# Performance work log

Hardware: AMD Instinct MI355X
Metric: run time of the kernel (lower is better)

Reference implementation:

```python
import jax, jax.numpy as jnp
import numpy as np

# dims: B batch, N nodes, E edges, C=dim_in, W=window_len, D=embed_dim, O=dim_out, K=link_len, NB=bootstrap count
B, N, E, C, W, D, O, K, NB = 16, 2000, 3000, 17, 12, 16, 256, 3, 3


def setup_inputs() -> dict:
    key = jax.random.key(0)
    ks = jax.random.split(key, 20)
    return {
        "x": jax.random.normal(ks[0], (B, N, C), jnp.float32),
        "x_window": jax.random.normal(ks[1], (B, W, N, 1), jnp.float32),
        "node_embeddings": jax.random.normal(ks[2], (N, D), jnp.float32) * 0.1,
        "fixed_adj": 0,
        "adj": jax.random.normal(ks[3], (N, N), jnp.float32),
        "stay_cost": 1,
        "jump_cost": 1,
        "ZFC_input": jax.random.normal(ks[4], (B, O // 8), jnp.float32),
        "hodge_Laplacian": jax.random.normal(ks[5], (E, E), jnp.float32) * 0.02,
        "x_e_window": jax.random.normal(ks[6], (B, W, E, 1), jnp.float32),
        "incidence_matrix": jax.random.normal(ks[7], (N, E), jnp.float32) * 0.02,
        "weights_pool": jax.random.normal(ks[8], (D, K, C, O // 4), jnp.float32) * 0.05,
        "window_weights_supra": jax.random.normal(ks[9], (D, 1, O // 8), jnp.float32) * 0.05,
        "window_weights_temporal": jax.random.normal(ks[10], (D, 1, O // 2), jnp.float32) * 0.05,
        "bias_pool": jax.random.normal(ks[11], (D, O), jnp.float32) * 0.05,
        "T_param": jax.random.normal(ks[12], (W,), jnp.float32) * 0.1,
        "lin_w": jax.random.normal(ks[13], (1, 1), jnp.float32),
        "lin_b": jax.random.normal(ks[14], (1,), jnp.float32),
        "gnn_w": jax.random.normal(ks[15], (N, N), jnp.float32) * 0.02,
        "gnn_b": jnp.zeros((N,), jnp.float32),
        "bootstrap_idx": jnp.sort(jax.random.randint(ks[16], (NB,), 0, W)),
    }


def _forward(x, x_window, ne, fixed_adj, adj, stay_cost, jump_cost, ZFC_input,
             hodge, x_e_window, inc, wp, wws_p, wwt_p, bp, Tp, lin_w, lin_b,
             gnn_w, gnn_b, bidx):
    n = ne.shape[0]
    e = hodge.shape[0]
    b = x.shape[0]
    nb = bidx.shape[0]

    # adaptive transition matrix S (diag filled with stay_cost after relu)
    S0 = jax.nn.relu(ne @ ne.T)
    ii = jnp.arange(n)
    S0 = S0.at[ii, ii].set(jnp.float32(stay_cost))
    if fixed_adj:  # static Python bool branch
        S = adj * jnp.exp(S0)
    else:
        S = jax.nn.softmax(S0, axis=1)
    # faithful to torch broadcasting: column j divided by row-sum of row j
    S = S / jnp.sum(S, axis=1)

    # diffusion support power series: [I, S, S@S, ...]
    sup = [jnp.eye(n, dtype=S.dtype), S]
    for _ in range(2, K):
        sup.append(S @ sup[-1])
    supports = jnp.stack(sup, axis=0)  # (K, N, N)

    # supra-Laplacian: hodge on diagonal blocks, jump_cost*I on strict upper blocks
    supra = (jnp.kron(jnp.eye(nb, dtype=hodge.dtype), hodge)
             + jnp.kron(jnp.triu(jnp.ones((nb, nb), hodge.dtype), 1),
                        jnp.float32(jump_cost) * jnp.eye(e, dtype=hodge.dtype)))  # (nb*E, nb*E)

    # adaptive weights/bias from node embeddings
    weights = jnp.einsum('nd,dkio->nkio', ne, wp)   # (N, K, C, O/4)
    bias = ne @ bp                                   # (N, O)

    # graph diffusion branch
    x_s = jnp.einsum('knm,bmc->bknc', supports, x).transpose(0, 2, 1, 3)  # (B,N,K,C)
    x_sconv = jnp.einsum('bnki,nkio->bno', x_s, weights)                   # (B,N,O/4)

    # supra / hypergraph branch
    wws = jnp.einsum('nd,dio->nio', ne, wws_p)                 # (N,1,O/8)
    xe = x_e_window[:, bidx].reshape(b, nb * e, 1)             # bootstrap gather
    xe = xe * lin_w[0, 0] + lin_b[0]                           # Linear(1,1)
    xes = jnp.einsum('bmi,mn->bni', xe, supra).reshape(b, nb, 1, e)
    xen = jnp.einsum('bfim,mn->bfin', xes, inc.T).reshape(b, nb, n, 1)
    x_e_n_wconv = jnp.einsum('bfni,nio->bfno', xen, wws).mean(axis=1)  # (B,N,O/8)

    # temporal window branch (einsum fuses the permute + matmul with T)
    wwt = jnp.einsum('nd,dio->nio', ne, wwt_p)                  # (N,1,O/2)
    x_wconv_t = jnp.einsum('btni,nio,t->bno', x_window, wwt, Tp)  # (B,N,O/2)

    # ZFC branch: repeat over nodes, GNN = Linear(N,N) + relu, reshape (view) back
    ZFC = jnp.tile(ZFC_input.reshape(b, -1, 1), (1, 1, n))      # (B,O/8,N)
    zout = jax.nn.relu(ZFC @ gnn_w.T + gnn_b)                   # (B,O/8,N)
    x_ZFC = zout.reshape(b, n, -1)                              # (B,N,O/8) (reshape, not transpose)

    return jnp.concatenate([x_sconv, x_ZFC, x_wconv_t, x_e_n_wconv], axis=-1) + bias


def reference(x, x_window, node_embeddings, fixed_adj, adj, stay_cost, jump_cost,
              ZFC_input, hodge_Laplacian, x_e_window, incidence_matrix,
              weights_pool, window_weights_supra, window_weights_temporal,
              bias_pool, T_param, lin_w, lin_b, gnn_w, gnn_b, bootstrap_idx):
    return _forward(x, x_window, node_embeddings, fixed_adj, adj, stay_cost,
                    jump_cost, ZFC_input, hodge_Laplacian, x_e_window,
                    incidence_matrix, weights_pool, window_weights_supra,
                    window_weights_temporal, bias_pool, T_param, lin_w, lin_b,
                    gnn_w, gnn_b, bootstrap_idx)
```

## Files before the change

kernel.cpp:

```cpp
#include <hip/hip_runtime.h>
#include <hip/hip_bf16.h>

typedef __hip_bfloat16 bf16;
typedef unsigned short ushort_t;
typedef __attribute__((ext_vector_type(8))) short short8;
typedef __attribute__((ext_vector_type(4))) short short4_t;
typedef __attribute__((ext_vector_type(4))) float f32x4;
typedef __attribute__((ext_vector_type(2))) float f32x2;

#define B_ 16
#define N_ 2000
#define E_ 3000
#define C_ 17
#define W_ 12
#define D_ 16
#define O_ 256
#define NB_ 3
#define KPAD 2048
#define KI_ 51
#define SEGS 75
#define ECH 40
#define EPAD 768
#define JB 48

static __device__ __forceinline__ ushort_t f2b(float f) {
  bf16 h = __float2bfloat16(f);
  return *reinterpret_cast<ushort_t*>(&h);
}
static __device__ __forceinline__ float b2f_u(ushort_t u) {
  bf16 h = *reinterpret_cast<bf16*>(&u);
  return __bfloat162float(h);
}
__device__ __forceinline__ int idxval(const int* p, int i) {
  int iv = p[i];
  if (iv >= 0 && iv < 1000000) return iv;
  return (int)__int_as_float(iv);
}

__global__ void k_S(const float* __restrict__ ne, const int* __restrict__ stay,
                    ushort_t* __restrict__ S) {
  const int i = blockIdx.x;
  const int i2 = i + 1024;
  const int t = threadIdx.x;
  __shared__ float ne_l[512*20];
  __shared__ float reds[4], reds2[4];
  const bool has2 = (i2 < N_);
  f32x4 nei[4], nei2[4];
#pragma unroll
  for (int q = 0; q < 4; ++q) {
    nei[q] = *(const f32x4*)(ne + i*16 + q*4);
    nei2[q] = has2 ? *(const f32x4*)(ne + (long)i2*16 + q*4) : (f32x4){0.f,0.f,0.f,0.f};
  }
  const float stayf = (float)(*stay);
  float vals[8], vals2[8];
  float s = 0.f, s2 = 0.f;
  for (int c = 0; c < 4; ++c) {
    __syncthreads();
#pragma unroll
    for (int u = 0; u < 8; ++u) {
      int unit = t + u*256;
      int row = unit >> 2, dq = unit & 3;
      int gj = c*512 + row;
      f32x4 v = {0.f,0.f,0.f,0.f};
      if (gj < N_) v = *(const f32x4*)(ne + (long)gj*16 + dq*4);
      *(f32x4*)(ne_l + row*20 + dq*4) = v;
    }
    __syncthreads();
#pragma unroll
    for (int r = 0; r < 2; ++r) {
      int row_l = t + r*256;
      int j = c*512 + row_l;
      float e = 0.f, e2 = 0.f;
      if (j < N_) {
        f32x4 a4 = {0.f,0.f,0.f,0.f}, b4 = {0.f,0.f,0.f,0.f};
#pragma unroll
        for (int q = 0; q < 4; ++q) {
          f32x4 nl = *(const f32x4*)(ne_l + row_l*20 + q*4);
          a4 += nei[q]*nl;
          b4 += nei2[q]*nl;
        }
        float dot = a4.x + a4.y + a4.z + a4.w;
        float v = dot > 0.f ? dot : 0.f;
        if (j == i) v = stayf;
        e = __expf(v);
        s += e;
        if (has2) {
          float dot2 = b4.x + b4.y + b4.z + b4.w;
          float v2 = dot2 > 0.f ? dot2 : 0.f;
          if (j == i2) v2 = stayf;
          e2 = __expf(v2);
          s2 += e2;
        }
      }
      vals[2*c + r] = e;
      vals2[2*c + r] = e2;
    }
  }
#pragma unroll
  for (int off = 32; off > 0; off >>= 1) {
    s  += __shfl_xor(s,  off, 64);
    s2 += __shfl_xor(s2, off, 64);
  }
  if ((t & 63) == 0) { reds[t >> 6] = s; reds2[t >> 6] = s2; }
  __syncthreads();
  s  = reds[0] + reds[1] + reds[2] + reds[3];
  s2 = reds2[0] + reds2[1] + reds2[2] + reds2[3];
  const float inv = 1.f/s;
  const float inv2 = has2 ? 1.f/s2 : 0.f;
#pragma unroll
  for (int it = 0; it < 8; ++it) {
    int j = t + it*256;
    S[(long)i*KPAD + j] = f2b(vals[it]*inv);
    S[(long)i2*KPAD + j] = has2 ? f2b(vals2[it]*inv2) : (ushort_t)0;
  }
}

__global__ void k_small(const float* __restrict__ xew, const int* __restrict__ bidx,
                        const float* __restrict__ lw, const float* __restrict__ lb,
                        const int* __restrict__ jc, float* __restrict__ u,
                        float* __restrict__ v,
                        const float* __restrict__ xwin, const float* __restrict__ Tp,
                        float* __restrict__ xw,
                        const float* __restrict__ gw, float* __restrict__ g,
                        const float* __restrict__ x, ushort_t* __restrict__ BT1,
                        const float* __restrict__ ne, const float* __restrict__ wp,
                        const float* __restrict__ bp, ushort_t* __restrict__ Wd) {
  const int bid = blockIdx.x;
  const int t = threadIdx.x;
  if (bid < 188) {
    int idx = bid*256 + t;
    if (idx >= B_*E_) return;
    int b = idx / E_, e = idx - b*E_;
    const float lwf = lw[0], lbf = lb[0];
    float uu = 0.f, vv = 0.f;
#pragma unroll
    for (int f = 0; f < NB_; ++f) {
      int tt = idxval(bidx, f);
      if (tt < 0) tt = 0;
      if (tt >= W_) tt = W_ - 1;
      float val = xew[(b*W_ + tt)*E_ + e]*lwf + lbf;
      uu += val;
      vv += (float)(NB_ - 1 - f)*val;
    }
    u[idx] = uu;
    v[idx] = vv*(float)(*jc);
  } else if (bid < 313) {
    int idx = (bid - 188)*256 + t;
    int b = idx / N_, n = idx - b*N_;
    float s = 0.f;
#pragma unroll
    for (int tt = 0; tt < W_; ++tt) s += xwin[(b*W_ + tt)*N_ + n]*Tp[tt];
    xw[idx] = s;
  } else if (bid < 2313) {
    int i = bid - 313;
    float s = 0.f;
    for (int j4 = t*4; j4 < N_; j4 += 1024) {
      f32x4 vv = *(const f32x4*)(gw + (long)i*N_ + j4);
      s += vv.x + vv.y + vv.z + vv.w;
    }
#pragma unroll
    for (int off = 32; off > 0; off >>= 1) s += __shfl_xor(s, off, 64);
    __shared__ float red[4];
    if ((t & 63) == 0) red[t >> 6] = s;
    __syncthreads();
    if (t == 0) g[i] = red[0] + red[1] + red[2] + red[3];
  } else if (bid < 2601) {
    int j = bid - 2313;
    int bb = j / C_, cc = j - bb*C_;
#pragma unroll
    for (int uu = 0; uu < 8; ++uu) {
      int n = t + uu*256;
      float vv = 0.f;
      if (bb < B_ && n < N_) vv = x[(bb*N_ + n)*C_ + cc];
      BT1[(long)j*KPAD + n] = f2b(vv);
    }
  } else {
    __shared__ float wp_l[16][256];
    __shared__ float ne_l[40][16];
    int w = bid - 2601;
    int c0 = (w % 13) * 256;
    int n0 = (w / 13) * 40;
    int c = c0 + t;
    int ki = c >> 6, o = c & 63;
#pragma unroll
    for (int d = 0; d < 16; ++d)
      wp_l[d][t] = (ki < KI_) ? wp[d*3264 + c] : bp[d*256 + o];
    for (int i = t; i < 40*16; i += 256)
      ne_l[i >> 4][i & 15] = ne[(long)(n0 + (i >> 4))*16 + (i & 15)];
    __syncthreads();
    float wreg[16];
#pragma unroll
    for (int d = 0; d < 16; ++d) wreg[d] = wp_l[d][t];
    ushort_t* wout = Wd + (long)n0*3328 + c;
    for (int n = 0; n < 40; ++n) {
      f32x4 a4 = {0.f,0.f,0.f,0.f};
#pragma unroll
      for (int q = 0; q < 4; ++q) {
        f32x4 nv = *(const f32x4*)&ne_l[n][q*4];
        a4.x += nv.x*wreg[q*4+0];
        a4.y += nv.y*wreg[q*4+1];
        a4.z += nv.z*wreg[q*4+2];
        a4.w += nv.w*wreg[q*4+3];
      }
      wout[(long)n*3328] = f2b(a4.x + a4.y + a4.z + a4.w);
    }
  }
}

__global__ __launch_bounds__(256) void k_mm2(const ushort_t* __restrict__ A,
                                             const ushort_t* __restrict__ BT,
                                             float* __restrict__ Cf,
                                             ushort_t* __restrict__ Cb,
                                             int writeCb) {
  __shared__ ushort_t lds[3][4096];
  const int t = threadIdx.x;
  const int m0 = blockIdx.x * 16;
  const int j0 = blockIdx.y * JB;
  const int wv = t >> 6, lane = t & 63;
  const int lm = lane & 15, lg = lane >> 4;
  const char* gA = (const char*)A + (size_t)m0 * (KPAD*2);
  const char* gB = (const char*)BT + (size_t)j0 * (KPAD*2);

  f32x4 acc = {0.f,0.f,0.f,0.f};

  auto stage = [&](int p, int s) {
    const long kb = (long)s * 128;
#pragma unroll
    for (int u = 0; u < 2; ++u) {
      int x = (u*256 + t) << 4;
      int y = x ^ (((x >> 7) & 7) << 4);
      int r = y >> 7, c = y & 127;
      const char* gp = (r < 16) ? gA + (long)r*(KPAD*2) + kb + c
                                : gB + (long)(r-16)*(KPAD*2) + kb + c;
      __builtin_amdgcn_global_load_lds(
          (const __attribute__((address_space(1))) void*)gp,
          (__attribute__((address_space(3))) void*)(&lds[p][u*2048 + wv*512]),
          16, 0, 0);
    }
  };

  auto compute = [&](int p) {
    if (wv < 3) {
      const char* base = (const char*)&lds[p][0];
#pragma unroll
      for (int kg = 0; kg < 2; ++kg) {
        int xA = (lm << 7) + (kg << 6) + (lg << 4);
        xA ^= ((xA >> 7) & 7) << 4;
        short8 a = *(const short8*)(base + xA);
        int xB = ((16 + wv*16 + lm) << 7) + (kg << 6) + (lg << 4);
        xB ^= ((xB >> 7) & 7) << 4;
        short8 b = *(const short8*)(base + xB);
        acc = __builtin_amdgcn_mfma_f32_16x16x32_bf16(a, b, acc, 0, 0, 0);
      }
    }
  };

  stage(0, 0);
  stage(1, 1);
  for (int s = 0; s < 32; ++s) {
    int p = s % 3;
    if (s < 30) {
      stage((s + 2) % 3, s + 2);
      asm volatile("s_waitcnt vmcnt(4)" ::: "memory");
    } else if (s == 30) {
      asm volatile("s_waitcnt vmcnt(2)" ::: "memory");
    } else {
      asm volatile("s_waitcnt vmcnt(0)" ::: "memory");
    }
    __builtin_amdgcn_s_barrier();
    asm volatile("" ::: "memory");
    compute(p);
    asm volatile("" ::: "memory");
    __builtin_amdgcn_s_barrier();
  }

  if (wv < 3) {
    int j = j0 + wv*16 + lm;
    int m = m0 + lg*4;
    *(f32x4*)(Cf + (long)j*KPAD + m) = acc;
    if (writeCb) {
      short4_t hv;
#pragma unroll
      for (int q = 0; q < 4; ++q)
        hv[q] = (m + q < N_) ? (short)f2b(acc[q]) : (short)0;
      *(short4_t*)(Cb + (long)j*KPAD + m) = hv;
    }
  }
}

__global__ void k_hodge(const float* __restrict__ u, const float* __restrict__ hodge,
                        float* __restrict__ xesP) {
  const int t = threadIdx.x;
  const int e2 = blockIdx.x*256 + t;
  const int seg = blockIdx.y;
  const int e1a = seg*ECH;
  __shared__ float ul[ECH*16];
  for (int idx = t; idx < ECH*16; idx += 256) {
    int bb = idx / ECH, ee = idx - bb*ECH;
    ul[ee*16 + bb] = u[bb*E_ + e1a + ee];
  }
  __syncthreads();
  if (e2 >= E_) return;
  float acc[16] = {};
  for (int ee = 0; ee < ECH; ee += 8) {
    float h[8];
#pragma unroll
    for (int q = 0; q < 8; ++q) h[q] = hodge[(long)(e1a + ee + q)*E_ + e2];
#pragma unroll
    for (int q = 0; q < 8; ++q) {
#pragma unroll
      for (int g4 = 0; g4 < 4; ++g4) {
        f32x4 u4 = *(const f32x4*)&ul[(ee + q)*16 + g4*4];
        acc[g4*4+0] += u4.x*h[q];
        acc[g4*4+1] += u4.y*h[q];
        acc[g4*4+2] += u4.z*h[q];
        acc[g4*4+3] += u4.w*h[q];
      }
    }
  }
#pragma unroll
  for (int bb = 0; bb < 16; ++bb)
    xesP[((long)seg*16 + bb)*E_ + e2] = acc[bb];
}

__global__ void k_redxes(const float* __restrict__ xesP, const float* __restrict__ v,
                         float* __restrict__ xes) {
  int idx = blockIdx.x*256 + threadIdx.x;
  if (idx >= B_*E_) return;
  int b = idx / E_, e = idx - b*E_;
  float s = v[idx];
#pragma unroll 15
  for (int q = 0; q < SEGS; ++q) s += xesP[((long)q*16 + b)*E_ + e];
  xes[idx] = s;
}

__global__ __launch_bounds__(256) void k_inc(const float* __restrict__ xes,
                                             const float* __restrict__ inc,
                                             float* __restrict__ xenP) {
  __shared__ float xes_l[16*EPAD];
  const int t = threadIdx.x;
  const int wv = t >> 6, lane = t & 63;
  const int cy = blockIdx.y;
  const int n0 = blockIdx.x*8;
  for (int i4 = t; i4 < 16*(EPAD/4); i4 += 256) {
    int row = i4 / (EPAD/4);
    int el = (i4 - row*(EPAD/4)) << 2;
    int e = cy*EPAD + el;
    f32x4 vv = {0.f,0.f,0.f,0.f};
    if (e < E_) vv = *(const f32x4*)(xes + (long)row*E_ + e);
    *(f32x4*)&xes_l[row*EPAD + el] = vv;
  }
  __syncthreads();
  const int na = n0 + wv*2;
  const int nb = na + 1;
  const float* rowA = inc + (long)na*E_ + cy*EPAD;
  const float* rowB = inc + (long)nb*E_ + cy*EPAD;
  float accA[16] = {}, accB[16] = {};
#pragma unroll
  for (int g = 0; g < 3; ++g) {
    int e4 = (g*64 + lane) << 2;
    bool ok = (cy*EPAD + e4) < E_;
    f32x4 ia = {0.f,0.f,0.f,0.f}, ib = {0.f,0.f,0.f,0.f};
    if (ok) { ia = *(const f32x4*)(rowA + e4); ib = *(const f32x4*)(rowB + e4); }
#pragma unroll
    for (int b = 0; b < 16; ++b) {
      f32x4 xs = *(const f32x4*)&xes_l[b*EPAD + e4];
      accA[b] += xs.x*ia.x + xs.y*ia.y + xs.z*ia.z + xs.w*ia.w;
      accB[b] += xs.x*ib.x + xs.y*ib.y + xs.z*ib.z + xs.w*ib.w;
    }
  }
#pragma unroll
  for (int b = 0; b < 16; ++b) {
#pragma unroll
    for (int off = 32; off > 0; off >>= 1) {
      accA[b] += __shfl_xor(accA[b], off, 64);
      accB[b] += __shfl_xor(accB[b], off, 64);
    }
  }
  const int bl = lane & 15;
  float oA = 0.f, oB = 0.f;
#pragma unroll
  for (int b = 0; b < 16; ++b)
    if (bl == b) { oA = accA[b]; oB = accB[b]; }
  if (lane < 16)
    xenP[((long)cy*16 + bl)*N_ + na] = oA*(1.f/3.f);
  else if (lane < 32)
    xenP[((long)cy*16 + bl)*N_ + nb] = oB*(1.f/3.f);
}

#define NT2 2
__global__ __launch_bounds__(256) void k_tailF(const float* __restrict__ x,
                          const float* __restrict__ C32a,
                          const float* __restrict__ C32b,
                          const ushort_t* __restrict__ Wd,
                          const float* __restrict__ ne,
                          const float* __restrict__ bp,
                          const float* __restrict__ wwt, const float* __restrict__ wws,
                          const float* __restrict__ zfc, const float* __restrict__ gnnb,
                          const float* __restrict__ g, const float* __restrict__ xw,
                          const float* __restrict__ xenP,
                          float* __restrict__ out) {
  __shared__ float xs_l[52*20];
  __shared__ float ne_l[NT2][16];
  __shared__ float wb[NT2][160];
  __shared__ float bi[NT2][192];
  __shared__ float gi_l[NT2][32], gb_l[NT2][32];
  __shared__ int   q_l[NT2][32];
  __shared__ float zf_l[16*32];
  __shared__ float xwv[16][NT2], xev[16][NT2];
  const int t = threadIdx.x;
  if (blockIdx.x < 2000) {
    const int n = blockIdx.x;
    const int lane = t & 63, wv = t >> 6;
    for (int idx = t; idx < KI_*16; idx += 256) {
      int ki = idx >> 4, b = idx & 15;
      int k = ki / C_, cc = ki - k*C_;
      float v;
      if (k == 0)      v = x[(b*N_ + n)*C_ + cc];
      else if (k == 1) v = C32a[(long)(b*C_ + cc)*KPAD + n];
      else             v = C32b[(long)(b*C_ + cc)*KPAD + n];
      xs_l[ki*20 + b] = v;
    }
    if (t < 16) xs_l[KI_*20 + t] = 1.0f;
    __syncthreads();
    const ushort_t* wrow = Wd + (long)n*3328 + lane;
    f32x4 acc = {0.f,0.f,0.f,0.f};
#pragma unroll
    for (int ki = 0; ki < 52; ++ki) {
      float w = b2f_u(wrow[ki*64]);
      f32x4 xs4 = *(const f32x4*)&xs_l[ki*20 + wv*4];
      acc += xs4 * w;
    }
#pragma unroll
    for (int j = 0; j < 4; ++j)
      out[((long)((wv*4 + j)*N_ + n))*O_ + lane] = acc[j];
  } else {
    const int n0 = (blockIdx.x - 2000)*NT2;
    zf_l[t] = zfc[t];
    zf_l[t + 256] = zfc[t + 256];
    if (t < NT2*16) ne_l[t >> 4][t & 15] = ne[(n0 + (t >> 4))*16 + (t & 15)];
    if (t < NT2*32) {
      int nl = t >> 5, j = t & 31;
      int flat = (n0 + nl)*32 + j;
      int q = flat / N_;
      int i = flat - q*N_;
      q_l[nl][j] = q;
      gi_l[nl][j] = g[i];
      gb_l[nl][j] = gnnb[i];
    }
    if (t < 16*NT2) {
      int b = t / NT2, nl = t - b*NT2;
      int n = n0 + nl;
      xwv[b][nl] = xw[b*N_ + n];
      xev[b][nl] = xenP[b*N_ + n] + xenP[(16 + b)*N_ + n]
                 + xenP[(32 + b)*N_ + n] + xenP[(48 + b)*N_ + n];
    }
    __syncthreads();
    for (int idx = t; idx < NT2*192; idx += 256) {
      int nl = idx / 192, op = idx - nl*192;
      float wv2 = 0.f, bv = 0.f;
#pragma unroll
      for (int d = 0; d < 16; ++d) {
        float nd = ne_l[nl][d];
        bv += nd * bp[d*256 + 64 + op];
        float ww = 0.f;
        if (op >= 32 && op < 160) ww = wwt[d*128 + (op - 32)];
        else if (op >= 160)       ww = wws[d*32 + (op - 160)];
        wv2 += nd * ww;
      }
      bi[nl][op] = bv;
      if (op >= 32) wb[nl][op - 32] = wv2;
    }
    __syncthreads();
    for (int idx = t; idx < 16*NT2*192; idx += 256) {
      int b = idx / (NT2*192);
      int r = idx - b*(NT2*192);
      int nl = r / 192, op = r - nl*192;
      float val;
      if (op < 32) {
        float z = zf_l[b*32 + q_l[nl][op]]*gi_l[nl][op] + gb_l[nl][op];
        val = z > 0.f ? z : 0.f;
      } else if (op < 160) {
        val = xwv[b][nl] * wb[nl][op - 32];
      } else {
        val = xev[b][nl] * wb[nl][op - 32];
      }
      out[((long)(b*N_ + n0 + nl))*O_ + 64 + op] = val + bi[nl][op];
    }
  }
}

extern "C" void kernel_launch(void* const* d_in, const int* in_sizes, int n_in,
                              void* d_out, int out_size, void* d_ws, size_t ws_size,
                              hipStream_t stream) {
  const float* x     = (const float*)d_in[0];
  const float* xwin  = (const float*)d_in[1];
  const float* ne    = (const float*)d_in[2];
  const int*   stay  = (const int*)d_in[5];
  const int*   jc    = (const int*)d_in[6];
  const float* zfc   = (const float*)d_in[7];
  const float* hodge = (const float*)d_in[8];
  const float* xew   = (const float*)d_in[9];
  const float* inc   = (const float*)d_in[10];
  const float* wp    = (const float*)d_in[11];
  const float* wws   = (const float*)d_in[12];
  const float* wwt   = (const float*)d_in[13];
  const float* bp    = (const float*)d_in[14];
  const float* Tp    = (const float*)d_in[15];
  const float* lw    = (const float*)d_in[16];
  const float* lb    = (const float*)d_in[17];
  const float* gw    = (const float*)d_in[18];
  const float* gnnb  = (const float*)d_in[19];
  const int*   bidx  = (const int*)d_in[20];
  float* out = (float*)d_out;

  char* wsb = (char*)d_ws;
  float*    C32a = (float*)(wsb);
  float*    C32b = (float*)(wsb + 2359296);
  ushort_t* BT1  = (ushort_t*)(wsb + 2359296);
  float* u    = (float*)(wsb + 4718592);
  float* v    = (float*)(wsb + 4910592);
  float* xes  = (float*)(wsb + 5102592);
  float* xw   = (float*)(wsb + 5294592);
  float* g    = (float*)(wsb + 5422592);
  float* xenP = (float*)(wsb + 5430592);
  ushort_t* Wd = (ushort_t*)(wsb + 5942592);

  char* ob = (char*)d_out;
  ushort_t* S    = (ushort_t*)(ob);
  ushort_t* BT2  = (ushort_t*)(ob + 8388608);
  float*    xesP = (float*)(ob + 9568256);

  k_small<<<3251, 256, 0, stream>>>(xew, bidx, lw, lb, jc, u, v,
                                    xwin, Tp, xw, gw, g, x, BT1,
                                    ne, wp, bp, Wd);
  k_S<<<1024, 256, 0, stream>>>(ne, stay, S);
  k_mm2<<<dim3(128,6), 256, 0, stream>>>(S, BT1, C32a, BT2, 1);
  k_mm2<<<dim3(128,6), 256, 0, stream>>>(S, BT2, C32b, nullptr, 0);
  k_hodge<<<dim3(12, SEGS), 256, 0, stream>>>(u, hodge, xesP);
  k_redxes<<<188, 256, 0, stream>>>(xesP, v, xes);
  k_inc<<<dim3(250, 4), 256, 0, stream>>>(xes, inc, xenP);
  k_tailF<<<3000, 256, 0, stream>>>(x, C32a, C32b, Wd, ne, bp, wwt, wws,
                                    zfc, gnnb, g, xw, xenP, out);
}
```

Measured before the change: 259.7 us.

## Merge independent stages into shared launches to overlap work and cut launch count

Folds the S softmax kernel into the preprocessing launch and pairs each bf16 matmul pass with independent work: the first with the Hodge product, the second with the xes reduction. Block index ranges pick which body runs, so the launch count drops from eight to five and independent stages can fill idle CUs together. In exchange, the combined kernels share one LDS allocation and register budget sized for the largest branch, which may lower occupancy for the lighter branches.

```diff
diff --git a/kernel.cpp b/kernel.cpp
--- a/kernel.cpp
+++ b/kernel.cpp
@@ -37,185 +37,14 @@
   return (int)__int_as_float(iv);
 }
 
-__global__ void k_S(const float* __restrict__ ne, const int* __restrict__ stay,
-                    ushort_t* __restrict__ S) {
-  const int i = blockIdx.x;
-  const int i2 = i + 1024;
+__device__ __forceinline__ void mm_body(int bx, int by,
+    const ushort_t* __restrict__ A, const ushort_t* __restrict__ BT,
+    float* __restrict__ Cf, ushort_t* __restrict__ Cb, int writeCb,
+    ushort_t* smem) {
+  ushort_t (*lds)[4096] = (ushort_t(*)[4096])smem;
   const int t = threadIdx.x;
-  __shared__ float ne_l[512*20];
-  __shared__ float reds[4], reds2[4];
-  const bool has2 = (i2 < N_);
-  f32x4 nei[4], nei2[4];
-#pragma unroll
-  for (int q = 0; q < 4; ++q) {
-    nei[q] = *(const f32x4*)(ne + i*16 + q*4);
-    nei2[q] = has2 ? *(const f32x4*)(ne + (long)i2*16 + q*4) : (f32x4){0.f,0.f,0.f,0.f};
-  }
-  const float stayf = (float)(*stay);
-  float vals[8], vals2[8];
-  float s = 0.f, s2 = 0.f;
-  for (int c = 0; c < 4; ++c) {
-    __syncthreads();
-#pragma unroll
-    for (int u = 0; u < 8; ++u) {
-      int unit = t + u*256;
-      int row = unit >> 2, dq = unit & 3;
-      int gj = c*512 + row;
-      f32x4 v = {0.f,0.f,0.f,0.f};
-      if (gj < N_) v = *(const f32x4*)(ne + (long)gj*16 + dq*4);
-      *(f32x4*)(ne_l + row*20 + dq*4) = v;
-    }
-    __syncthreads();
-#pragma unroll
-    for (int r = 0; r < 2; ++r) {
-      int row_l = t + r*256;
-      int j = c*512 + row_l;
-      float e = 0.f, e2 = 0.f;
-      if (j < N_) {
-        f32x4 a4 = {0.f,0.f,0.f,0.f}, b4 = {0.f,0.f,0.f,0.f};
-#pragma unroll
-        for (int q = 0; q < 4; ++q) {
-          f32x4 nl = *(const f32x4*)(ne_l + row_l*20 + q*4);
-          a4 += nei[q]*nl;
-          b4 += nei2[q]*nl;
-        }
-        float dot = a4.x + a4.y + a4.z + a4.w;
-        float v = dot > 0.f ? dot : 0.f;
-        if (j == i) v = stayf;
-        e = __expf(v);
-        s += e;
-        if (has2) {
-          float dot2 = b4.x + b4.y + b4.z + b4.w;
-          float v2 = dot2 > 0.f ? dot2 : 0.f;
-          if (j == i2) v2 = stayf;
-          e2 = __expf(v2);
-          s2 += e2;
-        }
-      }
-      vals[2*c + r] = e;
-      vals2[2*c + r] = e2;
-    }
-  }
-#pragma unroll
-  for (int off = 32; off > 0; off >>= 1) {
-    s  += __shfl_xor(s,  off, 64);
-    s2 += __shfl_xor(s2, off, 64);
-  }
-  if ((t & 63) == 0) { reds[t >> 6] = s; reds2[t >> 6] = s2; }
-  __syncthreads();
-  s  = reds[0] + reds[1] + reds[2] + reds[3];
-  s2 = reds2[0] + reds2[1] + reds2[2] + reds2[3];
-  const float inv = 1.f/s;
-  const float inv2 = has2 ? 1.f/s2 : 0.f;
-#pragma unroll
-  for (int it = 0; it < 8; ++it) {
-    int j = t + it*256;
-    S[(long)i*KPAD + j] = f2b(vals[it]*inv);
-    S[(long)i2*KPAD + j] = has2 ? f2b(vals2[it]*inv2) : (ushort_t)0;
-  }
-}
-
-__global__ void k_small(const float* __restrict__ xew, const int* __restrict__ bidx,
-                        const float* __restrict__ lw, const float* __restrict__ lb,
-                        const int* __restrict__ jc, float* __restrict__ u,
-                        float* __restrict__ v,
-                        const float* __restrict__ xwin, const float* __restrict__ Tp,
-                        float* __restrict__ xw,
-                        const float* __restrict__ gw, float* __restrict__ g,
-                        const float* __restrict__ x, ushort_t* __restrict__ BT1,
-                        const float* __restrict__ ne, const float* __restrict__ wp,
-                        const float* __restrict__ bp, ushort_t* __restrict__ Wd) {
-  const int bid = blockIdx.x;
-  const int t = threadIdx.x;
-  if (bid < 188) {
-    int idx = bid*256 + t;
-    if (idx >= B_*E_) return;
-    int b = idx / E_, e = idx - b*E_;
-    const float lwf = lw[0], lbf = lb[0];
-    float uu = 0.f, vv = 0.f;
-#pragma unroll
-    for (int f = 0; f < NB_; ++f) {
-      int tt = idxval(bidx, f);
-      if (tt < 0) tt = 0;
-      if (tt >= W_) tt = W_ - 1;
-      float val = xew[(b*W_ + tt)*E_ + e]*lwf + lbf;
-      uu += val;
-      vv += (float)(NB_ - 1 - f)*val;
-    }
-    u[idx] = uu;
-    v[idx] = vv*(float)(*jc);
-  } else if (bid < 313) {
-    int idx = (bid - 188)*256 + t;
-    int b = idx / N_, n = idx - b*N_;
-    float s = 0.f;
-#pragma unroll
-    for (int tt = 0; tt < W_; ++tt) s += xwin[(b*W_ + tt)*N_ + n]*Tp[tt];
-    xw[idx] = s;
-  } else if (bid < 2313) {
-    int i = bid - 313;
-    float s = 0.f;
-    for (int j4 = t*4; j4 < N_; j4 += 1024) {
-      f32x4 vv = *(const f32x4*)(gw + (long)i*N_ + j4);
-      s += vv.x + vv.y + vv.z + vv.w;
-    }
-#pragma unroll
-    for (int off = 32; off > 0; off >>= 1) s += __shfl_xor(s, off, 64);
-    __shared__ float red[4];
-    if ((t & 63) == 0) red[t >> 6] = s;
-    __syncthreads();
-    if (t == 0) g[i] = red[0] + red[1] + red[2] + red[3];
-  } else if (bid < 2601) {
-    int j = bid - 2313;
-    int bb = j / C_, cc = j - bb*C_;
-#pragma unroll
-    for (int uu = 0; uu < 8; ++uu) {
-      int n = t + uu*256;
-      float vv = 0.f;
-      if (bb < B_ && n < N_) vv = x[(bb*N_ + n)*C_ + cc];
-      BT1[(long)j*KPAD + n] = f2b(vv);
-    }
-  } else {
-    __shared__ float wp_l[16][256];
-    __shared__ float ne_l[40][16];
-    int w = bid - 2601;
-    int c0 = (w % 13) * 256;
-    int n0 = (w / 13) * 40;
-    int c = c0 + t;
-    int ki = c >> 6, o = c & 63;
-#pragma unroll
-    for (int d = 0; d < 16; ++d)
-      wp_l[d][t] = (ki < KI_) ? wp[d*3264 + c] : bp[d*256 + o];
-    for (int i = t; i < 40*16; i += 256)
-      ne_l[i >> 4][i & 15] = ne[(long)(n0 + (i >> 4))*16 + (i & 15)];
-    __syncthreads();
-    float wreg[16];
-#pragma unroll
-    for (int d = 0; d < 16; ++d) wreg[d] = wp_l[d][t];
-    ushort_t* wout = Wd + (long)n0*3328 + c;
-    for (int n = 0; n < 40; ++n) {
-      f32x4 a4 = {0.f,0.f,0.f,0.f};
-#pragma unroll
-      for (int q = 0; q < 4; ++q) {
-        f32x4 nv = *(const f32x4*)&ne_l[n][q*4];
-        a4.x += nv.x*wreg[q*4+0];
-        a4.y += nv.y*wreg[q*4+1];
-        a4.z += nv.z*wreg[q*4+2];
-        a4.w += nv.w*wreg[q*4+3];
-      }
-      wout[(long)n*3328] = f2b(a4.x + a4.y + a4.z + a4.w);
-    }
-  }
-}
-
-__global__ __launch_bounds__(256) void k_mm2(const ushort_t* __restrict__ A,
-                                             const ushort_t* __restrict__ BT,
-                                             float* __restrict__ Cf,
-                                             ushort_t* __restrict__ Cb,
-                                             int writeCb) {
-  __shared__ ushort_t lds[3][4096];
-  const int t = threadIdx.x;
-  const int m0 = blockIdx.x * 16;
-  const int j0 = blockIdx.y * JB;
+  const int m0 = bx * 16;
+  const int j0 = by * JB;
   const int wv = t >> 6, lane = t & 63;
   const int lm = lane & 15, lg = lane >> 4;
   const char* gA = (const char*)A + (size_t)m0 * (KPAD*2);
@@ -288,13 +117,12 @@
   }
 }
 
-__global__ void k_hodge(const float* __restrict__ u, const float* __restrict__ hodge,
-                        float* __restrict__ xesP) {
+__device__ __forceinline__ void hodge_body(int w, const float* __restrict__ u,
+    const float* __restrict__ hodge, float* __restrict__ xesP, float* ul) {
   const int t = threadIdx.x;
-  const int e2 = blockIdx.x*256 + t;
-  const int seg = blockIdx.y;
+  const int e2 = (w % 12)*256 + t;
+  const int seg = w / 12;
   const int e1a = seg*ECH;
-  __shared__ float ul[ECH*16];
   for (int idx = t; idx < ECH*16; idx += 256) {
     int bb = idx / ECH, ee = idx - bb*ECH;
     ul[ee*16 + bb] = u[bb*E_ + e1a + ee];
@@ -323,15 +151,202 @@
     xesP[((long)seg*16 + bb)*E_ + e2] = acc[bb];
 }
 
-__global__ void k_redxes(const float* __restrict__ xesP, const float* __restrict__ v,
-                         float* __restrict__ xes) {
-  int idx = blockIdx.x*256 + threadIdx.x;
-  if (idx >= B_*E_) return;
-  int b = idx / E_, e = idx - b*E_;
-  float s = v[idx];
+__global__ __launch_bounds__(256) void k_pre(
+    const float* __restrict__ xew, const int* __restrict__ bidx,
+    const float* __restrict__ lw, const float* __restrict__ lb,
+    const int* __restrict__ jc, float* __restrict__ u, float* __restrict__ v,
+    const float* __restrict__ xwin, const float* __restrict__ Tp,
+    float* __restrict__ xw, const float* __restrict__ gw, float* __restrict__ g,
+    const float* __restrict__ x, ushort_t* __restrict__ BT1,
+    const float* __restrict__ ne, const float* __restrict__ wp,
+    const float* __restrict__ bp, ushort_t* __restrict__ Wd,
+    const int* __restrict__ stay, ushort_t* __restrict__ S) {
+  __shared__ float smem[10248];
+  const int bid = blockIdx.x;
+  const int t = threadIdx.x;
+  if (bid < 188) {
+    int idx = bid*256 + t;
+    if (idx >= B_*E_) return;
+    int b = idx / E_, e = idx - b*E_;
+    const float lwf = lw[0], lbf = lb[0];
+    float uu = 0.f, vv = 0.f;
+#pragma unroll
+    for (int f = 0; f < NB_; ++f) {
+      int tt = idxval(bidx, f);
+      if (tt < 0) tt = 0;
+      if (tt >= W_) tt = W_ - 1;
+      float val = xew[(b*W_ + tt)*E_ + e]*lwf + lbf;
+      uu += val;
+      vv += (float)(NB_ - 1 - f)*val;
+    }
+    u[idx] = uu;
+    v[idx] = vv*(float)(*jc);
+  } else if (bid < 313) {
+    int idx = (bid - 188)*256 + t;
+    int b = idx / N_, n = idx - b*N_;
+    float s = 0.f;
+#pragma unroll
+    for (int tt = 0; tt < W_; ++tt) s += xwin[(b*W_ + tt)*N_ + n]*Tp[tt];
+    xw[idx] = s;
+  } else if (bid < 2313) {
+    int i = bid - 313;
+    float* red = smem;
+    float s = 0.f;
+    for (int j4 = t*4; j4 < N_; j4 += 1024) {
+      f32x4 vv = *(const f32x4*)(gw + (long)i*N_ + j4);
+      s += vv.x + vv.y + vv.z + vv.w;
+    }
+#pragma unroll
+    for (int off = 32; off > 0; off >>= 1) s += __shfl_xor(s, off, 64);
+    if ((t & 63) == 0) red[t >> 6] = s;
+    __syncthreads();
+    if (t == 0) g[i] = red[0] + red[1] + red[2] + red[3];
+  } else if (bid < 2601) {
+    int j = bid - 2313;
+    int bb = j / C_, cc = j - bb*C_;
+#pragma unroll
+    for (int uu = 0; uu < 8; ++uu) {
+      int n = t + uu*256;
+      float vv = 0.f;
+      if (bb < B_ && n < N_) vv = x[(bb*N_ + n)*C_ + cc];
+      BT1[(long)j*KPAD + n] = f2b(vv);
+    }
+  } else if (bid < 3251) {
+    float (*wp_l)[256] = (float(*)[256])smem;
+    float (*ne_l)[16]  = (float(*)[16])(smem + 4096);
+    int w = bid - 2601;
+    int c0 = (w % 13) * 256;
+    int n0 = (w / 13) * 40;
+    int c = c0 + t;
+    int ki = c >> 6, o = c & 63;
+#pragma unroll
+    for (int d = 0; d < 16; ++d)
+      wp_l[d][t] = (ki < KI_) ? wp[d*3264 + c] : bp[d*256 + o];
+    for (int i = t; i < 40*16; i += 256)
+      ne_l[i >> 4][i & 15] = ne[(long)(n0 + (i >> 4))*16 + (i & 15)];
+    __syncthreads();
+    float wreg[16];
+#pragma unroll
+    for (int d = 0; d < 16; ++d) wreg[d] = wp_l[d][t];
+    ushort_t* wout = Wd + (long)n0*3328 + c;
+    for (int n = 0; n < 40; ++n) {
+      f32x4 a4 = {0.f,0.f,0.f,0.f};
+#pragma unroll
+      for (int q = 0; q < 4; ++q) {
+        f32x4 nv = *(const f32x4*)&ne_l[n][q*4];
+        a4.x += nv.x*wreg[q*4+0];
+        a4.y += nv.y*wreg[q*4+1];
+        a4.z += nv.z*wreg[q*4+2];
+        a4.w += nv.w*wreg[q*4+3];
+      }
+      wout[(long)n*3328] = f2b(a4.x + a4.y + a4.z + a4.w);
+    }
+  } else {
+    float* ne_l = smem;
+    float* reds = smem + 10240;
+    float* reds2 = smem + 10244;
+    const int i = bid - 3251;
+    const int i2 = i + 1024;
+    const bool has2 = (i2 < N_);
+    f32x4 nei[4], nei2[4];
+#pragma unroll
+    for (int q = 0; q < 4; ++q) {
+      nei[q] = *(const f32x4*)(ne + i*16 + q*4);
+      nei2[q] = has2 ? *(const f32x4*)(ne + (long)i2*16 + q*4) : (f32x4){0.f,0.f,0.f,0.f};
+    }
+    const float stayf = (float)(*stay);
+    float vals[8], vals2[8];
+    float s = 0.f, s2 = 0.f;
+    for (int c = 0; c < 4; ++c) {
+      __syncthreads();
+#pragma unroll
+      for (int uu = 0; uu < 8; ++uu) {
+        int unit = t + uu*256;
+        int row = unit >> 2, dq = unit & 3;
+        int gj = c*512 + row;
+        f32x4 vv = {0.f,0.f,0.f,0.f};
+        if (gj < N_) vv = *(const f32x4*)(ne + (long)gj*16 + dq*4);
+        *(f32x4*)(ne_l + row*20 + dq*4) = vv;
+      }
+      __syncthreads();
+#pragma unroll
+      for (int r = 0; r < 2; ++r) {
+        int row_l = t + r*256;
+        int j = c*512 + row_l;
+        float e = 0.f, e2 = 0.f;
+        if (j < N_) {
+          f32x4 a4 = {0.f,0.f,0.f,0.f}, b4 = {0.f,0.f,0.f,0.f};
+#pragma unroll
+          for (int q = 0; q < 4; ++q) {
+            f32x4 nl = *(const f32x4*)(ne_l + row_l*20 + q*4);
+            a4 += nei[q]*nl;
+            b4 += nei2[q]*nl;
+          }
+          float dot = a4.x + a4.y + a4.z + a4.w;
+          float vv = dot > 0.f ? dot : 0.f;
+          if (j == i) vv = stayf;
+          e = __expf(vv);
+          s += e;
+          if (has2) {
+            float dot2 = b4.x + b4.y + b4.z + b4.w;
+            float v2 = dot2 > 0.f ? dot2 : 0.f;
+            if (j == i2) v2 = stayf;
+            e2 = __expf(v2);
+            s2 += e2;
+          }
+        }
+        vals[2*c + r] = e;
+        vals2[2*c + r] = e2;
+      }
+    }
+#pragma unroll
+    for (int off = 32; off > 0; off >>= 1) {
+      s  += __shfl_xor(s,  off, 64);
+      s2 += __shfl_xor(s2, off, 64);
+    }
+    if ((t & 63) == 0) { reds[t >> 6] = s; reds2[t >> 6] = s2; }
+    __syncthreads();
+    s  = reds[0] + reds[1] + reds[2] + reds[3];
+    s2 = reds2[0] + reds2[1] + reds2[2] + reds2[3];
+    const float inv = 1.f/s;
+    const float inv2 = has2 ? 1.f/s2 : 0.f;
+#pragma unroll
+    for (int it = 0; it < 8; ++it) {
+      int j = t + it*256;
+      S[(long)i*KPAD + j] = f2b(vals[it]*inv);
+      S[(long)i2*KPAD + j] = has2 ? f2b(vals2[it]*inv2) : (ushort_t)0;
+    }
+  }
+}
+
+__global__ __launch_bounds__(256) void k_mmh(const ushort_t* __restrict__ A,
+    const ushort_t* __restrict__ BT1, float* __restrict__ C32a,
+    ushort_t* __restrict__ BT2,
+    const float* __restrict__ u, const float* __restrict__ hodge,
+    float* __restrict__ xesP) {
+  __shared__ ushort_t smem[3*4096];
+  const int bid = blockIdx.x;
+  if (bid < 768) mm_body(bid & 127, bid >> 7, A, BT1, C32a, BT2, 1, smem);
+  else           hodge_body(bid - 768, u, hodge, xesP, (float*)smem);
+}
+
+__global__ __launch_bounds__(256) void k_mmr(const ushort_t* __restrict__ A,
+    const ushort_t* __restrict__ BT2, float* __restrict__ C32b,
+    const float* __restrict__ xesP, const float* __restrict__ v,
+    float* __restrict__ xes) {
+  __shared__ ushort_t smem[3*4096];
+  const int bid = blockIdx.x;
+  if (bid < 768) {
+    mm_body(bid & 127, bid >> 7, A, BT2, C32b, nullptr, 0, smem);
+  } else {
+    int idx = (bid - 768)*256 + threadIdx.x;
+    if (idx >= B_*E_) return;
+    int b = idx / E_, e = idx - b*E_;
+    float s = v[idx];
 #pragma unroll 15
-  for (int q = 0; q < SEGS; ++q) s += xesP[((long)q*16 + b)*E_ + e];
-  xes[idx] = s;
+    for (int q = 0; q < SEGS; ++q) s += xesP[((long)q*16 + b)*E_ + e];
+    xes[idx] = s;
+  }
 }
 
 __global__ __launch_bounds__(256) void k_inc(const float* __restrict__ xes,
@@ -531,14 +546,11 @@
   ushort_t* BT2  = (ushort_t*)(ob + 8388608);
   float*    xesP = (float*)(ob + 9568256);
 
-  k_small<<<3251, 256, 0, stream>>>(xew, bidx, lw, lb, jc, u, v,
-                                    xwin, Tp, xw, gw, g, x, BT1,
-                                    ne, wp, bp, Wd);
-  k_S<<<1024, 256, 0, stream>>>(ne, stay, S);
-  k_mm2<<<dim3(128,6), 256, 0, stream>>>(S, BT1, C32a, BT2, 1);
-  k_mm2<<<dim3(128,6), 256, 0, stream>>>(S, BT2, C32b, nullptr, 0);
-  k_hodge<<<dim3(12, SEGS), 256, 0, stream>>>(u, hodge, xesP);
-  k_redxes<<<188, 256, 0, stream>>>(xesP, v, xes);
+  k_pre<<<4275, 256, 0, stream>>>(xew, bidx, lw, lb, jc, u, v,
+                                  xwin, Tp, xw, gw, g, x, BT1,
+                                  ne, wp, bp, Wd, stay, S);
+  k_mmh<<<1668, 256, 0, stream>>>(S, BT1, C32a, BT2, u, hodge, xesP);
+  k_mmr<<<956, 256, 0, stream>>>(S, BT2, C32b, xesP, v, xes);
   k_inc<<<dim3(250, 4), 256, 0, stream>>>(xes, inc, xenP);
   k_tailF<<<3000, 256, 0, stream>>>(x, C32a, C32b, Wd, ne, bp, wwt, wws,
                                     zfc, gnnb, g, xw, xenP, out);
```

New measurement: 251.0 us. 1.03x faster.
